# Kernel optimization log

Hardware: AMD Instinct MI355X
Metric: run time of the kernel (lower is better)

## Reference

```python
import jax, jax.numpy as jnp
import numpy as np

N_IN, N_OUT, N_TO = 64, 64, 16  # connection table: each output plane gets N_TO random input planes
K = N_OUT * N_TO                # 1024 connections
KH, KW = 3, 3
B, H, W = 4, 192, 192


def setup_inputs() -> dict:
    key = jax.random.key(0)
    kx, kw_, kb, kc = jax.random.split(key, 4)
    x = jax.random.normal(kx, (B, N_IN, H, W), dtype=jnp.float32)
    weight = jax.random.normal(kw_, (K, KH, KW), dtype=jnp.float32) * (1.0 / np.sqrt(KH * KW * N_TO))
    bias = jax.random.normal(kb, (N_OUT,), dtype=jnp.float32) * 0.01
    # maps.random semantics: each output plane j has exactly N_TO input connections
    conn_in = jax.random.randint(kc, (K,), 0, N_IN, dtype=jnp.int32)
    conn_out = jnp.repeat(jnp.arange(N_OUT, dtype=jnp.int32), N_TO)
    return {"x": x, "weight": weight, "bias": bias, "conn_in": conn_in, "conn_out": conn_out}


def reference(x, weight, bias, conn_in, conn_out):
    # x: [B, nIn, H, W]; weight: [K, kH, kW]; connection k convolves plane conn_in[k]
    # into plane conn_out[k] with its own kernel (valid conv, stride 1).
    nK = weight.shape[0]
    nOut = bias.shape[0]
    xg = x[:, conn_in]                       # [B, K, H, W] gather input planes per connection
    y = jax.lax.conv_general_dilated(
        xg, weight[:, None],                 # kernel [K, 1, kH, kW], grouped => per-connection conv
        window_strides=(1, 1), padding='VALID',
        feature_group_count=nK,
        dimension_numbers=('NCHW', 'OIHW', 'NCHW'))  # [B, K, Ho, Wo]
    # scatter-add connections into their output planes
    out = jax.ops.segment_sum(jnp.moveaxis(y, 1, 0), conn_out, num_segments=nOut)  # [nOut, B, Ho, Wo]
    return jnp.moveaxis(out, 0, 1) + bias[None, :, None, None]
```

## Files before the change

### kernel.cpp

```cpp
#include <hip/hip_runtime.h>
#include <hip/hip_bf16.h>

#define HH 192
#define WW 192
#define HOUT 190
#define NCH 64
#define W2_N (64 * 9 * 64)

typedef __attribute__((ext_vector_type(8))) short bf16x8;
typedef __attribute__((ext_vector_type(4))) float f32x4;

static __device__ __forceinline__ ushort f2bf(float f) {
    __hip_bfloat16 h = __float2bfloat16(f);
    return *reinterpret_cast<ushort*>(&h);
}

__global__ __launch_bounds__(256) void build_w2(const float* __restrict__ w,
                                                const int* __restrict__ conn,
                                                ushort* __restrict__ w2) {
    int idx = blockIdx.x * 256 + threadIdx.x;
    if (idx >= W2_N) return;
    int o = idx / 576, rem = idx - o * 576, tap = rem >> 6, c = rem & 63;
    float s = 0.f;
    #pragma unroll
    for (int t = 0; t < 16; ++t) {
        int k = o * 16 + t;
        if (conn[k] == c) s += w[k * 9 + tap];
    }
    w2[idx] = f2bf(s);
}

__global__ __launch_bounds__(256, 2) void scm_mfma(
    const float* __restrict__ x,
    const ushort* __restrict__ w2,
    const float* __restrict__ bias,
    float* __restrict__ out)
{
    __shared__ ushort xt[10 * 18 * 72];

    const int tid  = threadIdx.x;
    const int lane = tid & 63;
    const int wv   = tid >> 6;
    const int col  = lane & 15;
    const int g    = lane >> 4;

    const int bid = blockIdx.x;
    const int lid = (bid & 7) * 144 + (bid >> 3);
    const int b      = lid / 288;
    const int tileid = lid % 288;
    const int ti0 = (tileid / 12) * 8;
    const int tj0 = (tileid % 12) * 16;

    const ushort* bp = w2 + (16 * wv + col) * 576 + g * 8;
    bf16x8 Bf[9][2];
    #pragma unroll
    for (int tap = 0; tap < 9; ++tap)
        #pragma unroll
        for (int s = 0; s < 2; ++s)
            Bf[tap][s] = *(const bf16x8*)(bp + tap * 64 + s * 32);

    {
        const int srr  = lane / 18;
        const int scol = lane - srr * 18;
        const bool act = lane < 54;
        int gc = tj0 + scol; if (gc > 191) gc = 191;
        int gr0 = ti0 + srr;     if (gr0 > 191) gr0 = 191;
        int gr1 = ti0 + srr + 3; if (gr1 > 191) gr1 = 191;
        int gr2 = ti0 + srr + 6; if (gr2 > 191) gr2 = 191;
        int gr3 = ti0 + srr + 9; if (gr3 > 191) gr3 = 191;

        float vals[16][4];
        #pragma unroll
        for (int j = 0; j < 16; ++j) {
            const int c = wv * 16 + j;
            const float* xc = x + ((size_t)(b * NCH + c)) * (HH * WW);
            vals[j][0] = xc[gr0 * WW + gc];
            vals[j][1] = xc[gr1 * WW + gc];
            vals[j][2] = xc[gr2 * WW + gc];
            vals[j][3] = xc[gr3 * WW + gc];
        }
        __builtin_amdgcn_sched_barrier(0);
        if (act) {
            #pragma unroll
            for (int j = 0; j < 16; ++j) {
                const int c = wv * 16 + j;
                xt[((srr    ) * 18 + scol) * 72 + c] = f2bf(vals[j][0]);
                xt[((srr + 3) * 18 + scol) * 72 + c] = f2bf(vals[j][1]);
                xt[((srr + 6) * 18 + scol) * 72 + c] = f2bf(vals[j][2]);
                if (srr == 0)
                    xt[(9 * 18 + scol) * 72 + c] = f2bf(vals[j][3]);
            }
        }
    }
    __syncthreads();

    f32x4 acc[8];
    #pragma unroll
    for (int i = 0; i < 8; ++i) acc[i] = (f32x4){0.f, 0.f, 0.f, 0.f};

    const ushort* ap0 = &xt[col * 72 + g * 8];

    #pragma unroll
    for (int s = 0; s < 2; ++s) {
        #pragma unroll
        for (int kw = 0; kw < 3; ++kw) {
            bf16x8 f[10];
            #pragma unroll
            for (int R = 0; R < 10; ++R)
                f[R] = *(const bf16x8*)(ap0 + (R * 18 + kw) * 72 + s * 32);
            __builtin_amdgcn_sched_barrier(0);
            #pragma unroll
            for (int Mt = 0; Mt < 8; ++Mt) {
                acc[Mt] = __builtin_amdgcn_mfma_f32_16x16x32_bf16(Bf[kw][s],     f[Mt],     acc[Mt], 0, 0, 0);
                acc[Mt] = __builtin_amdgcn_mfma_f32_16x16x32_bf16(Bf[3 + kw][s], f[Mt + 1], acc[Mt], 0, 0, 0);
                acc[Mt] = __builtin_amdgcn_mfma_f32_16x16x32_bf16(Bf[6 + kw][s], f[Mt + 2], acc[Mt], 0, 0, 0);
            }
        }
    }

    const int pcol = tj0 + col;
    const int obase = 16 * wv + 4 * g;
    float bv[4];
    #pragma unroll
    for (int reg = 0; reg < 4; ++reg) bv[reg] = bias[obase + reg];

    if (pcol < HOUT) {
        #pragma unroll
        for (int Mt = 0; Mt < 8; ++Mt) {
            const int row = ti0 + Mt;
            if (row < HOUT) {
                float* rp = out + ((size_t)(b * NCH + obase) * HOUT + row) * HOUT + pcol;
                #pragma unroll
                for (int reg = 0; reg < 4; ++reg)
                    rp[(size_t)reg * HOUT * HOUT] = acc[Mt][reg] + bv[reg];
            }
        }
    }
}

extern "C" void kernel_launch(void* const* d_in, const int* in_sizes, int n_in,
                              void* d_out, int out_size, void* d_ws, size_t ws_size,
                              hipStream_t stream) {
    const float* x       = (const float*)d_in[0];
    const float* weight  = (const float*)d_in[1];
    const float* bias    = (const float*)d_in[2];
    const int*   conn_in = (const int*)d_in[3];

    ushort* w2 = (ushort*)d_ws;

    build_w2<<<dim3((W2_N + 255) / 256), dim3(256), 0, stream>>>(weight, conn_in, w2);

    scm_mfma<<<dim3(1152), dim3(256), 0, stream>>>(x, w2, bias, (float*)d_out);
}
```

Measured before the change: 34.88 us.

## Cut register pressure to fit three blocks per CU in sparse conv MFMA kernel

Raises the launch-bounds occupancy target from 2 to 3 blocks per CU. To make room, the staging loads are split into two passes of 8 channels, and the weight fragments are loaded per K-half instead of being held for the whole kernel. Pairs of bf16 values are packed into 32-bit LDS stores, which halves the store count. The aim is more latency hiding of global loads, at the cost of less load-level parallelism per pass and weight loads sitting inside the compute loop.

```diff
diff --git a/kernel.cpp b/kernel.cpp
--- a/kernel.cpp
+++ b/kernel.cpp
@@ -13,6 +13,9 @@
 static __device__ __forceinline__ ushort f2bf(float f) {
     __hip_bfloat16 h = __float2bfloat16(f);
     return *reinterpret_cast<ushort*>(&h);
+}
+static __device__ __forceinline__ uint pack2bf(float lo, float hi) {
+    return (uint)f2bf(lo) | ((uint)f2bf(hi) << 16);
 }
 
 __global__ __launch_bounds__(256) void build_w2(const float* __restrict__ w,
@@ -30,7 +33,7 @@
     w2[idx] = f2bf(s);
 }
 
-__global__ __launch_bounds__(256, 2) void scm_mfma(
+__global__ __launch_bounds__(256, 3) void scm_mfma(
     const float* __restrict__ x,
     const ushort* __restrict__ w2,
     const float* __restrict__ bias,
@@ -51,14 +54,6 @@
     const int ti0 = (tileid / 12) * 8;
     const int tj0 = (tileid % 12) * 16;
 
-    const ushort* bp = w2 + (16 * wv + col) * 576 + g * 8;
-    bf16x8 Bf[9][2];
-    #pragma unroll
-    for (int tap = 0; tap < 9; ++tap)
-        #pragma unroll
-        for (int s = 0; s < 2; ++s)
-            Bf[tap][s] = *(const bf16x8*)(bp + tap * 64 + s * 32);
-
     {
         const int srr  = lane / 18;
         const int scol = lane - srr * 18;
@@ -69,26 +64,33 @@
         int gr2 = ti0 + srr + 6; if (gr2 > 191) gr2 = 191;
         int gr3 = ti0 + srr + 9; if (gr3 > 191) gr3 = 191;
 
-        float vals[16][4];
         #pragma unroll
-        for (int j = 0; j < 16; ++j) {
-            const int c = wv * 16 + j;
-            const float* xc = x + ((size_t)(b * NCH + c)) * (HH * WW);
-            vals[j][0] = xc[gr0 * WW + gc];
-            vals[j][1] = xc[gr1 * WW + gc];
-            vals[j][2] = xc[gr2 * WW + gc];
-            vals[j][3] = xc[gr3 * WW + gc];
-        }
-        __builtin_amdgcn_sched_barrier(0);
-        if (act) {
+        for (int pass = 0; pass < 2; ++pass) {
+            float v[8][4];
             #pragma unroll
-            for (int j = 0; j < 16; ++j) {
-                const int c = wv * 16 + j;
-                xt[((srr    ) * 18 + scol) * 72 + c] = f2bf(vals[j][0]);
-                xt[((srr + 3) * 18 + scol) * 72 + c] = f2bf(vals[j][1]);
-                xt[((srr + 6) * 18 + scol) * 72 + c] = f2bf(vals[j][2]);
-                if (srr == 0)
-                    xt[(9 * 18 + scol) * 72 + c] = f2bf(vals[j][3]);
+            for (int pj = 0; pj < 8; ++pj) {
+                const int c = wv * 16 + pass * 8 + pj;
+                const float* xc = x + ((size_t)(b * NCH + c)) * (HH * WW);
+                v[pj][0] = xc[gr0 * WW + gc];
+                v[pj][1] = xc[gr1 * WW + gc];
+                v[pj][2] = xc[gr2 * WW + gc];
+                v[pj][3] = xc[gr3 * WW + gc];
+            }
+            __builtin_amdgcn_sched_barrier(0);
+            if (act) {
+                #pragma unroll
+                for (int pp = 0; pp < 4; ++pp) {
+                    const int c = wv * 16 + pass * 8 + 2 * pp;
+                    uint k0 = pack2bf(v[2 * pp][0], v[2 * pp + 1][0]);
+                    uint k1 = pack2bf(v[2 * pp][1], v[2 * pp + 1][1]);
+                    uint k2 = pack2bf(v[2 * pp][2], v[2 * pp + 1][2]);
+                    uint k3 = pack2bf(v[2 * pp][3], v[2 * pp + 1][3]);
+                    *(uint*)&xt[((srr    ) * 18 + scol) * 72 + c] = k0;
+                    *(uint*)&xt[((srr + 3) * 18 + scol) * 72 + c] = k1;
+                    *(uint*)&xt[((srr + 6) * 18 + scol) * 72 + c] = k2;
+                    if (srr == 0)
+                        *(uint*)&xt[(9 * 18 + scol) * 72 + c] = k3;
+                }
             }
         }
     }
@@ -99,9 +101,14 @@
     for (int i = 0; i < 8; ++i) acc[i] = (f32x4){0.f, 0.f, 0.f, 0.f};
 
     const ushort* ap0 = &xt[col * 72 + g * 8];
+    const ushort* bp  = w2 + (16 * wv + col) * 576 + g * 8;
 
     #pragma unroll
     for (int s = 0; s < 2; ++s) {
+        bf16x8 Bs[9];
+        #pragma unroll
+        for (int tap = 0; tap < 9; ++tap)
+            Bs[tap] = *(const bf16x8*)(bp + tap * 64 + s * 32);
         #pragma unroll
         for (int kw = 0; kw < 3; ++kw) {
             bf16x8 f[10];
@@ -111,9 +118,9 @@
             __builtin_amdgcn_sched_barrier(0);
             #pragma unroll
             for (int Mt = 0; Mt < 8; ++Mt) {
-                acc[Mt] = __builtin_amdgcn_mfma_f32_16x16x32_bf16(Bf[kw][s],     f[Mt],     acc[Mt], 0, 0, 0);
-                acc[Mt] = __builtin_amdgcn_mfma_f32_16x16x32_bf16(Bf[3 + kw][s], f[Mt + 1], acc[Mt], 0, 0, 0);
-                acc[Mt] = __builtin_amdgcn_mfma_f32_16x16x32_bf16(Bf[6 + kw][s], f[Mt + 2], acc[Mt], 0, 0, 0);
+                acc[Mt] = __builtin_amdgcn_mfma_f32_16x16x32_bf16(Bs[kw],     f[Mt],     acc[Mt], 0, 0, 0);
+                acc[Mt] = __builtin_amdgcn_mfma_f32_16x16x32_bf16(Bs[3 + kw], f[Mt + 1], acc[Mt], 0, 0, 0);
+                acc[Mt] = __builtin_amdgcn_mfma_f32_16x16x32_bf16(Bs[6 + kw], f[Mt + 2], acc[Mt], 0, 0, 0);
             }
         }
     }
```

New measurement: 34.55 us. About the same (-0.9%).
